# Kernel optimization log

Measured on AMD Instinct MI355X. Metric: run time of the kernel, lower is better.

## Reference

```python
import jax, jax.numpy as jnp
import numpy as np

HW, B, C, NH, NC, HF, WF = 2500, 2, 256, 8, 6, 64, 176
DFF = 4 * C
EPS = 1e-5

def _layernorm(x, g, b):
    m = x.mean(-1, keepdims=True)
    v = ((x - m) ** 2).mean(-1, keepdims=True)
    return (x - m) / jnp.sqrt(v + EPS) * g + b

def _mha(q, kv, in_w, in_b, ow, ob):
    # q: [L,B,C], kv: [S,B,C] (batch_first=False, torch nn.MultiheadAttention)
    L, Bq, Cq = q.shape
    S = kv.shape[0]
    Dh = Cq // NH
    qp = (q @ in_w[:Cq].T + in_b[:Cq]).reshape(L, Bq, NH, Dh)
    kp = (kv @ in_w[Cq:2 * Cq].T + in_b[Cq:2 * Cq]).reshape(S, Bq, NH, Dh)
    vp = (kv @ in_w[2 * Cq:].T + in_b[2 * Cq:]).reshape(S, Bq, NH, Dh)
    att = jnp.einsum('lbhd,sbhd->bhls', qp, kp) * (1.0 / np.sqrt(Dh))
    att = jax.nn.softmax(att, axis=-1)
    out = jnp.einsum('bhls,sbhd->lbhd', att, vp).reshape(L, Bq, Cq)
    return out @ ow.T + ob

def _grid_sample_zeros(feat, grid):
    # feat: [B,N,C,H,W], grid: [B,N,Q,2] in [-1,1]; bilinear, align_corners=False, zero padding
    Bb, N, Cc, Hf, Wf = feat.shape
    Q = grid.shape[2]
    x = (grid[..., 0] + 1.0) * (Wf / 2.0) - 0.5
    y = (grid[..., 1] + 1.0) * (Hf / 2.0) - 0.5
    x0 = jnp.floor(x); y0 = jnp.floor(y)
    wx = x - x0; wy = y - y0
    x0i = x0.astype(jnp.int32); y0i = y0.astype(jnp.int32)
    ff = feat.reshape(Bb, N, Cc, Hf * Wf)
    def corner(xi, yi, w):
        valid = (xi >= 0) & (xi < Wf) & (yi >= 0) & (yi < Hf)
        idx = jnp.clip(yi, 0, Hf - 1) * Wf + jnp.clip(xi, 0, Wf - 1)  # [B,N,Q]
        g = jnp.take_along_axis(ff, jnp.broadcast_to(idx[:, :, None, :], (Bb, N, Cc, Q)), axis=-1)
        return g * (w * valid)[:, :, None, :]
    return (corner(x0i, y0i, (1.0 - wx) * (1.0 - wy)) + corner(x0i + 1, y0i, wx * (1.0 - wy))
            + corner(x0i, y0i + 1, (1.0 - wx) * wy) + corner(x0i + 1, y0i + 1, wx * wy))

def _forward(bev_queries, prev_bev, image_feat, reference_points, camera_intrinsics, camera_extrinsics,
             in_proj_w, in_proj_b, out_proj_w, out_proj_b, tsa_norm_g, tsa_norm_b,
             sca_w, sca_b, sca_norm_g, sca_norm_b, ffn_w1, ffn_b1, ffn_w2, ffn_b2, ffn_norm_g, ffn_norm_b):
    # TSA (dropout is identity in eval)
    tsa_out = _mha(bev_queries, prev_bev, in_proj_w, in_proj_b, out_proj_w, out_proj_b)
    x = _layernorm(bev_queries + tsa_out, tsa_norm_g, tsa_norm_b)
    # SCA: ego->camera->image projection
    R = camera_extrinsics[:, :, :3, :3]            # [B,N,3,3]
    t = camera_extrinsics[:, :, :3, 3]             # [B,N,3]
    R_e2c = jnp.swapaxes(R, -1, -2)
    t_e2c = -jnp.einsum('bnij,bnj->bni', R_e2c, t)
    pts_cam = jnp.einsum('bnij,qj->bnqi', R_e2c, reference_points) + t_e2c[:, :, None, :]  # [B,N,Q,3]
    pts_img = jnp.einsum('bnij,bnqj->bnqi', camera_intrinsics, pts_cam)
    uv = pts_img[..., :2] / jnp.maximum(pts_img[..., 2:3], 1e-5)
    grid = jnp.stack([2.0 * uv[..., 0] / WF - 1.0, 2.0 * uv[..., 1] / HF - 1.0], axis=-1)  # [B,N,Q,2]
    Bq = bev_queries.shape[1]
    feat_r = image_feat.reshape(Bq, NC, C, HF, WF)
    sampled = _grid_sample_zeros(feat_r, grid).mean(axis=1)   # [B,C,Q]
    sampled = jnp.transpose(sampled, (2, 0, 1))               # [Q,B,C]
    sca_out = sampled @ sca_w.T + sca_b
    x = _layernorm(x + sca_out, sca_norm_g, sca_norm_b)
    # FFN (torch nn.GELU default = exact erf)
    h = jax.nn.gelu(x @ ffn_w1 + ffn_b1, approximate=False)
    ffn_out = h @ ffn_w2 + ffn_b2
    return _layernorm(x + ffn_out, ffn_norm_g, ffn_norm_b)

def setup_inputs():
    key = jax.random.key(0)
    ks = jax.random.split(key, 16)
    f = jnp.float32
    s = 0.02
    return {
        'bev_queries': jax.random.normal(ks[0], (HW, B, C), f),
        'prev_bev': jax.random.normal(ks[1], (HW, B, C), f),
        'image_feat': jax.random.normal(ks[2], (B * NC, C, HF, WF), f),
        'reference_points': jax.random.normal(ks[3], (HW, 3), f) * 20.0,
        'camera_intrinsics': jax.random.normal(ks[4], (B, NC, 3, 3), f),
        'camera_extrinsics': jax.random.normal(ks[5], (B, NC, 4, 4), f),
        'spatial_shapes': jnp.array([[HF, WF]], jnp.int32),
        'in_proj_w': jax.random.normal(ks[6], (3 * C, C), f) * s,
        'in_proj_b': jnp.zeros((3 * C,), f),
        'out_proj_w': jax.random.normal(ks[7], (C, C), f) * s,
        'out_proj_b': jnp.zeros((C,), f),
        'tsa_norm_g': jnp.ones((C,), f), 'tsa_norm_b': jnp.zeros((C,), f),
        'sca_w': jax.random.normal(ks[8], (C, C), f) * s,
        'sca_b': jnp.zeros((C,), f),
        'sca_norm_g': jnp.ones((C,), f), 'sca_norm_b': jnp.zeros((C,), f),
        'ffn_w1': jax.random.normal(ks[9], (C, DFF), f) * s,
        'ffn_b1': jnp.zeros((DFF,), f),
        'ffn_w2': jax.random.normal(ks[10], (DFF, C), f) * s,
        'ffn_b2': jnp.zeros((C,), f),
        'ffn_norm_g': jnp.ones((C,), f), 'ffn_norm_b': jnp.zeros((C,), f),
    }

def reference(bev_queries, prev_bev, image_feat, reference_points, camera_intrinsics, camera_extrinsics,
              in_proj_w, in_proj_b, out_proj_w, out_proj_b, tsa_norm_g, tsa_norm_b,
              sca_w, sca_b, sca_norm_g, sca_norm_b, ffn_w1, ffn_b1, ffn_w2, ffn_b2, ffn_norm_g, ffn_norm_b,
              spatial_shapes):
    return _forward(bev_queries, prev_bev, image_feat, reference_points, camera_intrinsics, camera_extrinsics,
                    in_proj_w, in_proj_b, out_proj_w, out_proj_b, tsa_norm_g, tsa_norm_b,
                    sca_w, sca_b, sca_norm_g, sca_norm_b, ffn_w1, ffn_b1, ffn_w2, ffn_b2, ffn_norm_g, ffn_norm_b)
```

## Files before the change

kernel.cpp:

```cpp
#include <hip/hip_runtime.h>

typedef unsigned short u16;
typedef __attribute__((ext_vector_type(8))) __bf16 bf8_t;
typedef __attribute__((ext_vector_type(4))) float f4_t;

union bf8u { u16 u[8]; bf8_t v; uint4 q; };

__device__ __forceinline__ float bf2f(u16 v) {
  return __uint_as_float(((unsigned int)v) << 16);
}
__device__ __forceinline__ u16 f2bf(float f) {
  union { __bf16 h; u16 u; } c;
  c.h = (__bf16)f;
  return c.u;
}
__device__ __forceinline__ float bflo(unsigned int w) { return __uint_as_float(w << 16); }
__device__ __forceinline__ float bfhi(unsigned int w) { return __uint_as_float(w & 0xFFFF0000u); }
__device__ __forceinline__ float ldf1(const void* p, size_t i, int isf32) {
  return isf32 ? ((const float*)p)[i] : bf2f(((const u16*)p)[i]);
}

#define LQ    2500
#define LQP   2560
#define BB    2
#define CC    256
#define NCC   6
#define HFF   64
#define WFF   176
#define DFF   1024
#define MROWS 5000

#define WB_UV   256
#define WB_WQKV 240256
#define WB_WOP  633472
#define WB_WSC  764544
#define WB_WF1  895616
#define WB_WF2  1419904
#define WB_S1   1944192
#define WB_S2   (WB_S1 + 2621440)
#define WB_S3   (WB_S2 + 2621440)
#define WB_VT   (WB_S3 + 2621440)
#define WB_H    WB_S2

__global__ void detect_k(const u16* __restrict__ rp, int* __restrict__ flag) {
  int bad = 0;
  for (int i = threadIdx.x; i < 7500; i += 64) {
    float v = bf2f(rp[i]);
    if (!(fabsf(v) < 1e6f)) bad = 1;
  }
  int anybad = __any(bad);
  if (threadIdx.x == 0) flag[0] = anybad ? 1 : 0;
}

struct WDesc {
  const void* src[6];
  u16* dst[6];
  int n[6];
  int mode[6];
  int Kd[6], Nd[6];
};
__global__ __launch_bounds__(256) void cvtw_k(WDesc d,
    const void* __restrict__ refp, const void* __restrict__ intr,
    const void* __restrict__ extr, float* __restrict__ uv,
    const int* __restrict__ flag) {
  const int df = flag[0];
  const int i = blockIdx.y;
  if (i == 6) {
    for (int idx = blockIdx.x * 256 + threadIdx.x; idx < BB * NCC * LQ; idx += gridDim.x * 256) {
      const int bc = idx / LQ;
      const int q = idx - bc * LQ;
      float R[3][3], tv[3], Kc[3][3], p[3];
#pragma unroll
      for (int a = 0; a < 3; ++a) {
#pragma unroll
        for (int j = 0; j < 3; ++j) {
          R[a][j] = ldf1(extr, bc*16 + a*4 + j, df);
          Kc[a][j] = ldf1(intr, bc*9 + a*3 + j, df);
        }
        tv[a] = ldf1(extr, bc*16 + a*4 + 3, df);
      }
#pragma unroll
      for (int j = 0; j < 3; ++j) p[j] = ldf1(refp, q*3 + j, df) - tv[j];
      float pc[3];
#pragma unroll
      for (int a = 0; a < 3; ++a) pc[a] = R[0][a]*p[0] + R[1][a]*p[1] + R[2][a]*p[2];
      float im[3];
#pragma unroll
      for (int a = 0; a < 3; ++a) im[a] = Kc[a][0]*pc[0] + Kc[a][1]*pc[1] + Kc[a][2]*pc[2];
      const float z = fmaxf(im[2], 1e-5f);
      uv[(size_t)idx*2 + 0] = im[0] / z - 0.5f;
      uv[(size_t)idx*2 + 1] = im[1] / z - 0.5f;
    }
    return;
  }
  const int n = d.n[i];
  for (int j = blockIdx.x * 256 + threadIdx.x; j < n; j += gridDim.x * 256) {
    if (d.mode[i] == 3) {
      if (df) {
        const float4 r = ((const float4*)d.src[i])[j];
        const unsigned int lo = (unsigned int)f2bf(r.x) | ((unsigned int)f2bf(r.y) << 16);
        const unsigned int hi = (unsigned int)f2bf(r.z) | ((unsigned int)f2bf(r.w) << 16);
        ((uint2*)d.dst[i])[j] = make_uint2(lo, hi);
      } else {
        ((uint2*)d.dst[i])[j] = ((const uint2*)d.src[i])[j];
      }
    } else if (d.mode[i] == 2) {
      const int row = j / (LQP - LQ), col = LQ + j % (LQP - LQ);
      d.dst[i][(size_t)row * LQP + col] = 0;
    } else {
      const int K = d.Kd[i], N = d.Nd[i];
      const int nn = j / K, kk = j - nn * K;
      d.dst[i][j] = f2bf(ldf1(d.src[i], (size_t)kk * N + nn, df));
    }
  }
}

template<int KTPL, int ACT, int NT>
__global__ __launch_bounds__(64) void gemm_nl(
    const u16* __restrict__ Xv, const u16* __restrict__ W,
    const void* __restrict__ bias,
    u16* __restrict__ Y, int M, int N, const int* __restrict__ flag)
{
  const int df = flag[0];
  const int lane = threadIdx.x;
  const int ln15 = lane & 15, l4 = lane >> 4;
  const int m0 = blockIdx.x * 16, n0 = blockIdx.y * (NT * 16);
  const int am = min(m0 + ln15, M - 1);

  f4_t acc[NT];
#pragma unroll
  for (int nt = 0; nt < NT; ++nt) acc[nt] = (f4_t){0.f, 0.f, 0.f, 0.f};

#pragma unroll 8
  for (int k0 = 0; k0 < KTPL; k0 += 32) {
    bf8u a;
    a.q = *(const uint4*)(Xv + (size_t)am * KTPL + k0 + l4 * 8);
#pragma unroll
    for (int nt = 0; nt < NT; ++nt) {
      bf8u b;
      b.q = *(const uint4*)&W[(size_t)(n0 + nt * 16 + ln15) * KTPL + k0 + l4 * 8];
      acc[nt] = __builtin_amdgcn_mfma_f32_16x16x32_bf16(a.v, b.v, acc[nt], 0, 0, 0);
    }
  }
#pragma unroll
  for (int nt = 0; nt < NT; ++nt) {
    const int gn = n0 + nt * 16 + ln15;
    const float bv = ldf1(bias, gn, df);
#pragma unroll
    for (int r = 0; r < 4; ++r) {
      const int gm = m0 + l4 * 4 + r;
      if (gm < M) {
        float x = acc[nt][r] + bv;
        if (ACT) x = 0.5f * x * (1.f + erff(x * 0.70710678118654752f));
        Y[(size_t)gm * N + gn] = f2bf(x);
      }
    }
  }
}

template<int KT, int RES, int TOOUT>
__global__ __launch_bounds__(256) void gemm_ln(
    const u16* __restrict__ Xv, const u16* __restrict__ W,
    const void* __restrict__ bias, const void* __restrict__ resv,
    const void* __restrict__ gw, const void* __restrict__ bw,
    void* __restrict__ Yv, int M, const int* __restrict__ flag)
{
  __shared__ float sR[4][16];
  const int df = flag[0];
  const int t = threadIdx.x;
  const int lane = t & 63, wn = t >> 6;
  const int ln15 = lane & 15, l4 = lane >> 4;
  const int m0 = blockIdx.x * 16;
  const int am = min(m0 + ln15, M - 1);

  f4_t acc[4];
#pragma unroll
  for (int nt = 0; nt < 4; ++nt) acc[nt] = (f4_t){0.f, 0.f, 0.f, 0.f};

#pragma unroll 8
  for (int k0 = 0; k0 < KT; k0 += 32) {
    bf8u a;
    a.q = *(const uint4*)(Xv + (size_t)am * KT + k0 + l4 * 8);
#pragma unroll
    for (int nt = 0; nt < 4; ++nt) {
      bf8u b;
      b.q = *(const uint4*)&W[(size_t)(wn * 64 + nt * 16 + ln15) * KT + k0 + l4 * 8];
      acc[nt] = __builtin_amdgcn_mfma_f32_16x16x32_bf16(a.v, b.v, acc[nt], 0, 0, 0);
    }
  }
  float x[4][4];
#pragma unroll
  for (int nt = 0; nt < 4; ++nt) {
    const int gn = wn * 64 + nt * 16 + ln15;
    const float bv = ldf1(bias, gn, df);
#pragma unroll
    for (int r = 0; r < 4; ++r) {
      const int gm = m0 + l4 * 4 + r;
      float xx = acc[nt][r] + bv;
      const size_t ri = (size_t)min(gm, M - 1) * CC + gn;
      if (RES == 1)      xx += bf2f(((const u16*)resv)[ri]);
      else if (RES == 2) xx += ldf1(resv, ri, df);
      x[nt][r] = xx;
    }
  }
  float ps[4];
#pragma unroll
  for (int r = 0; r < 4; ++r) {
    ps[r] = x[0][r] + x[1][r] + x[2][r] + x[3][r];
#pragma unroll
    for (int o = 1; o < 16; o <<= 1) ps[r] += __shfl_xor(ps[r], o);
  }
  if (ln15 == 0) {
#pragma unroll
    for (int r = 0; r < 4; ++r) sR[wn][l4 * 4 + r] = ps[r];
  }
  __syncthreads();
  float mean[4];
#pragma unroll
  for (int r = 0; r < 4; ++r) {
    const int row = l4 * 4 + r;
    mean[r] = (sR[0][row] + sR[1][row] + sR[2][row] + sR[3][row]) * 0.00390625f;
  }
  __syncthreads();
  float pq[4];
#pragma unroll
  for (int r = 0; r < 4; ++r) {
    float d0 = x[0][r] - mean[r], d1 = x[1][r] - mean[r];
    float d2 = x[2][r] - mean[r], d3 = x[3][r] - mean[r];
    pq[r] = d0*d0 + d1*d1 + d2*d2 + d3*d3;
#pragma unroll
    for (int o = 1; o < 16; o <<= 1) pq[r] += __shfl_xor(pq[r], o);
  }
  if (ln15 == 0) {
#pragma unroll
    for (int r = 0; r < 4; ++r) sR[wn][l4 * 4 + r] = pq[r];
  }
  __syncthreads();
  float rstd[4];
#pragma unroll
  for (int r = 0; r < 4; ++r) {
    const int row = l4 * 4 + r;
    const float v = (sR[0][row] + sR[1][row] + sR[2][row] + sR[3][row]) * 0.00390625f;
    rstd[r] = rsqrtf(v + 1e-5f);
  }
#pragma unroll
  for (int nt = 0; nt < 4; ++nt) {
    const int gn = wn * 64 + nt * 16 + ln15;
    const float g = ldf1(gw, gn, df);
    const float be = ldf1(bw, gn, df);
#pragma unroll
    for (int r = 0; r < 4; ++r) {
      const int gm = m0 + l4 * 4 + r;
      if (gm < M) {
        const float y = (x[nt][r] - mean[r]) * rstd[r] * g + be;
        if (TOOUT && df) ((float*)Yv)[(size_t)gm * CC + gn] = y;
        else             ((u16*)Yv)[(size_t)gm * CC + gn] = f2bf(y);
      }
    }
  }
}

__global__ __launch_bounds__(64) void gemm_qkv(
    const void* __restrict__ Xq, const void* __restrict__ Xkv,
    const u16* __restrict__ Wqkv, const void* __restrict__ bias,
    u16* __restrict__ Qo, u16* __restrict__ Ko, u16* __restrict__ Vt,
    const int* __restrict__ flag)
{
  const int df = flag[0];
  const int lane = threadIdx.x;
  const int ln15 = lane & 15, l4 = lane >> 4;
  const int which = blockIdx.y >> 2;
  const int n0 = (blockIdx.y & 3) * 64;
  const void* Xv = (which == 0) ? Xq : Xkv;
  const u16* W = Wqkv + (size_t)which * 65536;
  const int m0 = blockIdx.x * 16;
  const int am = min(m0 + ln15, MROWS - 1);

  f4_t acc[4];
#pragma unroll
  for (int nt = 0; nt < 4; ++nt) acc[nt] = (f4_t){0.f, 0.f, 0.f, 0.f};

#pragma unroll 8
  for (int k0 = 0; k0 < CC; k0 += 32) {
    bf8u a;
    if (df) {
      const float* p = (const float*)Xv + (size_t)am * CC + k0 + l4 * 8;
      float4 r0 = *(const float4*)p, r1 = *(const float4*)(p + 4);
      a.u[0]=f2bf(r0.x); a.u[1]=f2bf(r0.y); a.u[2]=f2bf(r0.z); a.u[3]=f2bf(r0.w);
      a.u[4]=f2bf(r1.x); a.u[5]=f2bf(r1.y); a.u[6]=f2bf(r1.z); a.u[7]=f2bf(r1.w);
    } else {
      a.q = *(const uint4*)((const u16*)Xv + (size_t)am * CC + k0 + l4 * 8);
    }
#pragma unroll
    for (int nt = 0; nt < 4; ++nt) {
      bf8u b;
      b.q = *(const uint4*)&W[(size_t)(n0 + nt * 16 + ln15) * CC + k0 + l4 * 8];
      acc[nt] = __builtin_amdgcn_mfma_f32_16x16x32_bf16(a.v, b.v, acc[nt], 0, 0, 0);
    }
  }
#pragma unroll
  for (int nt = 0; nt < 4; ++nt) {
    const int gn = n0 + nt * 16 + ln15;
    const float bv = ldf1(bias, which * 256 + gn, df);
#pragma unroll
    for (int r = 0; r < 4; ++r) {
      const int gm = m0 + l4 * 4 + r;
      if (gm < MROWS) {
        const float x = acc[nt][r] + bv;
        if (which == 2) {
          const int tt = gm >> 1;
          const int tx = tt & 63;
          const int tp = (tx & 35) | ((tx & 12) << 1) | ((tx & 16) >> 2);
          Vt[(size_t)(gn + (gm & 1) * 256) * LQP + ((tt & ~63) | tp)] = f2bf(x);
        } else {
          u16* Y = (which == 0) ? Qo : Ko;
          Y[(size_t)gm * CC + gn] = f2bf(x);
        }
      }
    }
  }
}

#define TPW 10
__global__ __launch_bounds__(256) void attn_mf(
    const u16* __restrict__ Qw, const u16* __restrict__ Kw,
    const u16* __restrict__ Vt, u16* __restrict__ Ow)
{
  __shared__ float sO[4][16][33];
  __shared__ float sM[4][16];
  __shared__ float sL[4][16];
  const int t = threadIdx.x;
  const int lane = t & 63, w = t >> 6;
  const int ln15 = lane & 15, l4 = lane >> 4;
  const int q0 = blockIdx.x * 16;
  const int by = blockIdx.y;
  const int b = by >> 3, h = by & 7;
  const float SCL2E = 0.25505654481f;

  bf8u aq;
  {
    const int qrow = min(q0 + ln15, LQ - 1);
    bf8u qr; qr.q = *(const uint4*)&Qw[((size_t)qrow * BB + b) * CC + h * 32 + l4 * 8];
#pragma unroll
    for (int i = 0; i < 8; ++i) aq.u[i] = f2bf(bf2f(qr.u[i]) * SCL2E);
  }

  f4_t oacc[2];
  oacc[0] = (f4_t){0.f,0.f,0.f,0.f};
  oacc[1] = (f4_t){0.f,0.f,0.f,0.f};
  float m_r = -1e30f;
  float l_r = 0.f;

  const int kt0 = w * TPW;
  const u16* Kbase = &Kw[(size_t)b * CC + h * 32 + l4 * 8];
  const u16* Vbase = &Vt[(size_t)(by * 32 + ln15) * LQP + l4 * 8];

  bf8u bkn[4];
#pragma unroll
  for (int nt = 0; nt < 4; ++nt)
    bkn[nt].q = *(const uint4*)&Kbase[(size_t)(kt0 * 64 + nt * 16 + ln15) * CC];

  for (int kt = kt0; kt < kt0 + TPW; ++kt) {
    const int kb = kt * 64;
    bf8u av[2][2];
#pragma unroll
    for (int m = 0; m < 2; ++m)
#pragma unroll
      for (int dt = 0; dt < 2; ++dt)
        av[m][dt].q = *(const uint4*)&Vbase[(size_t)(dt * 16) * LQP + kb + m * 32];
    bf8u bk[4];
#pragma unroll
    for (int nt = 0; nt < 4; ++nt) bk[nt] = bkn[nt];
    if (kt + 1 < kt0 + TPW) {
#pragma unroll
      for (int nt = 0; nt < 4; ++nt)
        bkn[nt].q = *(const uint4*)&Kbase[(size_t)(kb + 64 + nt * 16 + ln15) * CC];
    }
    f4_t sv[4];
    __builtin_amdgcn_s_setprio(1);
#pragma unroll
    for (int nt = 0; nt < 4; ++nt) {
      f4_t z = (f4_t){0.f,0.f,0.f,0.f};
      sv[nt] = __builtin_amdgcn_mfma_f32_16x16x32_bf16(bk[nt].v, aq.v, z, 0, 0, 0);
    }
    __builtin_amdgcn_s_setprio(0);
    float p[4][4];
    if (kb + 64 <= LQ) {
#pragma unroll
      for (int nt = 0; nt < 4; ++nt)
#pragma unroll
        for (int r = 0; r < 4; ++r) p[nt][r] = sv[nt][r];
    } else {
#pragma unroll
      for (int nt = 0; nt < 4; ++nt)
#pragma unroll
        for (int r = 0; r < 4; ++r)
          p[nt][r] = (kb + nt * 16 + l4 * 4 + r < LQ) ? sv[nt][r] : -1e30f;
    }
    const float thr = m_r + 8.f;
    bool nd = false;
#pragma unroll
    for (int nt = 0; nt < 4; ++nt)
#pragma unroll
      for (int r = 0; r < 4; ++r) nd |= (p[nt][r] > thr);
    if (__any(nd)) {
      const float m0 = fmaxf(fmaxf(p[0][0], p[0][1]), fmaxf(p[0][2], p[0][3]));
      const float m1 = fmaxf(fmaxf(p[1][0], p[1][1]), fmaxf(p[1][2], p[1][3]));
      const float m2 = fmaxf(fmaxf(p[2][0], p[2][1]), fmaxf(p[2][2], p[2][3]));
      const float m3 = fmaxf(fmaxf(p[3][0], p[3][1]), fmaxf(p[3][2], p[3][3]));
      float mloc = fmaxf(fmaxf(m0, m1), fmaxf(m2, m3));
      mloc = fmaxf(mloc, __shfl_xor(mloc, 16));
      mloc = fmaxf(mloc, __shfl_xor(mloc, 32));
      const float mn = fmaxf(m_r, mloc);
      const float alpha = __builtin_amdgcn_exp2f(m_r - mn);
      m_r = mn;
      l_r *= alpha;
#pragma unroll
      for (int r = 0; r < 4; ++r) { oacc[0][r] *= alpha; oacc[1][r] *= alpha; }
    }
    float s = 0.f;
#pragma unroll
    for (int nt = 0; nt < 4; ++nt) {
#pragma unroll
      for (int r = 0; r < 4; ++r) {
        const float e = __builtin_amdgcn_exp2f(p[nt][r] - m_r);
        p[nt][r] = e; s += e;
      }
    }
    l_r += s;
    __builtin_amdgcn_s_setprio(1);
#pragma unroll
    for (int m = 0; m < 2; ++m) {
      bf8u pb;
#pragma unroll
      for (int i = 0; i < 8; ++i) pb.u[i] = f2bf(p[2 * m + (i >> 2)][i & 3]);
#pragma unroll
      for (int dt = 0; dt < 2; ++dt)
        oacc[dt] = __builtin_amdgcn_mfma_f32_16x16x32_bf16(av[m][dt].v, pb.v, oacc[dt], 0, 0, 0);
    }
    __builtin_amdgcn_s_setprio(0);
  }
  l_r += __shfl_xor(l_r, 16);
  l_r += __shfl_xor(l_r, 32);
#pragma unroll
  for (int dt = 0; dt < 2; ++dt)
#pragma unroll
    for (int r = 0; r < 4; ++r)
      sO[w][ln15][dt * 16 + l4 * 4 + r] = oacc[dt][r];
  if (l4 == 0) { sM[w][ln15] = m_r; sL[w][ln15] = l_r; }
  __syncthreads();
#pragma unroll
  for (int i = t; i < 512; i += 256) {
    const int row = i >> 5, col = i & 31;
    const float M = fmaxf(fmaxf(sM[0][row], sM[1][row]), fmaxf(sM[2][row], sM[3][row]));
    float l = 0.f, O = 0.f;
#pragma unroll
    for (int w4 = 0; w4 < 4; ++w4) {
      const float sc = __builtin_amdgcn_exp2f(sM[w4][row] - M);
      l += sc * sL[w4][row];
      O += sc * sO[w4][row][col];
    }
    const int q = q0 + row;
    if (q < LQ)
      Ow[((size_t)q * BB + b) * CC + h * 32 + col] = f2bf(O / l);
  }
}

__global__ __launch_bounds__(256) void samp_k(
    const void* __restrict__ feat, const float* __restrict__ uv,
    u16* __restrict__ S, const int* __restrict__ flag)
{
  const int df = flag[0];
  const int c = blockIdx.x;
  const int b = blockIdx.y / 5;
  const int ch = blockIdx.y % 5;
  const int qend = min((ch + 1) * 500, LQ);
  for (int q = ch * 500 + threadIdx.x; q < qend; q += 256) {
    float acc = 0.f;
#pragma unroll
    for (int cam = 0; cam < NCC; ++cam) {
      const int bc = b * NCC + cam;
      const float x = uv[((size_t)bc * LQ + q) * 2 + 0];
      const float y = uv[((size_t)bc * LQ + q) * 2 + 1];
      const float xf = floorf(x), yf = floorf(y);
      const int x0 = (int)xf, y0 = (int)yf;
      const float wx = x - xf, wy = y - yf;
      const size_t base = ((size_t)bc * CC + c) * (HFF * WFF);
      const bool vx0 = (x0 >= 0) & (x0 < WFF);
      const bool vx1 = (x0 + 1 >= 0) & (x0 + 1 < WFF);
      const bool vy0 = (y0 >= 0) & (y0 < HFF);
      const bool vy1 = (y0 + 1 >= 0) & (y0 + 1 < HFF);
      if (vy0) {
        const size_t rb = base + (size_t)y0 * WFF;
        if (vx0) acc += (1.f - wx) * (1.f - wy) * ldf1(feat, rb + x0, df);
        if (vx1) acc += wx * (1.f - wy) * ldf1(feat, rb + x0 + 1, df);
      }
      if (vy1) {
        const size_t rb = base + (size_t)(y0 + 1) * WFF;
        if (vx0) acc += (1.f - wx) * wy * ldf1(feat, rb + x0, df);
        if (vx1) acc += wx * wy * ldf1(feat, rb + x0 + 1, df);
      }
    }
    S[((size_t)q * BB + b) * CC + c] = f2bf(acc * (1.f / 6.f));
  }
}

extern "C" void kernel_launch(void* const* d_in, const int* in_sizes, int n_in,
                              void* d_out, int out_size, void* d_ws, size_t ws_size,
                              hipStream_t stream) {
  (void)in_sizes; (void)n_in; (void)out_size; (void)ws_size;
  char* base = (char*)d_ws;
  int* flag = (int*)base;
  float* UV = (float*)(base + WB_UV);
  u16* WQKV = (u16*)(base + WB_WQKV);
  u16* WOP  = (u16*)(base + WB_WOP);
  u16* WSC  = (u16*)(base + WB_WSC);
  u16* WF1  = (u16*)(base + WB_WF1);
  u16* WF2  = (u16*)(base + WB_WF2);
  u16* S1 = (u16*)(base + WB_S1);
  u16* S2 = (u16*)(base + WB_S2);
  u16* S3 = (u16*)(base + WB_S3);
  u16* VT = (u16*)(base + WB_VT);
  u16* H  = (u16*)(base + WB_H);

  detect_k<<<1, 64, 0, stream>>>((const u16*)d_in[3], flag);

  WDesc wd;
  wd.src[0] = d_in[7];  wd.dst[0] = WQKV; wd.n[0] = 49152;  wd.mode[0] = 3; wd.Kd[0] = 0;    wd.Nd[0] = 0;
  wd.src[1] = d_in[9];  wd.dst[1] = WOP;  wd.n[1] = 16384;  wd.mode[1] = 3; wd.Kd[1] = 0;    wd.Nd[1] = 0;
  wd.src[2] = d_in[13]; wd.dst[2] = WSC;  wd.n[2] = 16384;  wd.mode[2] = 3; wd.Kd[2] = 0;    wd.Nd[2] = 0;
  wd.src[3] = d_in[17]; wd.dst[3] = WF1;  wd.n[3] = 262144; wd.mode[3] = 1; wd.Kd[3] = 256;  wd.Nd[3] = 1024;
  wd.src[4] = d_in[19]; wd.dst[4] = WF2;  wd.n[4] = 262144; wd.mode[4] = 1; wd.Kd[4] = 1024; wd.Nd[4] = 256;
  wd.src[5] = nullptr;  wd.dst[5] = VT;   wd.n[5] = 512 * (LQP - LQ); wd.mode[5] = 2; wd.Kd[5] = 0; wd.Nd[5] = 0;
  cvtw_k<<<dim3(128, 7), 256, 0, stream>>>(wd, d_in[3], d_in[4], d_in[5], UV, flag);

  gemm_qkv<<<dim3(313, 12), 64, 0, stream>>>(d_in[0], d_in[1], WQKV, d_in[8], S1, S2, VT, flag);

  attn_mf<<<dim3(157, 16), 256, 0, stream>>>(S1, S2, VT, S3);

  gemm_ln<256,2,0><<<313, 256, 0, stream>>>(S3, WOP, d_in[10], d_in[0], d_in[11], d_in[12], S2, MROWS, flag);

  samp_k<<<dim3(CC, BB * 5), 256, 0, stream>>>(d_in[2], UV, VT, flag);

  gemm_ln<256,1,0><<<313, 256, 0, stream>>>(VT, WSC, d_in[14], S2, d_in[15], d_in[16], S1, MROWS, flag);

  gemm_nl<256,1,4><<<dim3(313, 16), 64, 0, stream>>>(S1, WF1, d_in[18], H, MROWS, DFF, flag);
  gemm_ln<1024,1,1><<<313, 256, 0, stream>>>(H, WF2, d_in[20], S1, d_in[21], d_in[22], d_out, MROWS, flag);
}
```

Baseline: 503.7 us.

## Process two query tiles per attention block to reuse K/V loads

The attention kernel now handles 32 queries per block as two 16-row MFMA tiles that share each loaded K and V fragment. This halves the global K/V traffic per query and halves the grid size. The probability packing also switches to the packed bf16 conversion instruction. The cost is higher register pressure from duplicated accumulators and softmax state, and fewer blocks (79x16) to spread across the CUs.

```diff
diff --git a/kernel.cpp b/kernel.cpp
--- a/kernel.cpp
+++ b/kernel.cpp
@@ -18,6 +18,11 @@
 __device__ __forceinline__ float bfhi(unsigned int w) { return __uint_as_float(w & 0xFFFF0000u); }
 __device__ __forceinline__ float ldf1(const void* p, size_t i, int isf32) {
   return isf32 ? ((const float*)p)[i] : bf2f(((const u16*)p)[i]);
+}
+__device__ __forceinline__ unsigned int cvtpk(float lo, float hi) {
+  unsigned int w;
+  asm("v_cvt_pk_bf16_f32 %0, %1, %2" : "=v"(w) : "v"(lo), "v"(hi));
+  return w;
 }
 
 #define LQ    2500
@@ -326,30 +331,35 @@
     const u16* __restrict__ Qw, const u16* __restrict__ Kw,
     const u16* __restrict__ Vt, u16* __restrict__ Ow)
 {
-  __shared__ float sO[4][16][33];
-  __shared__ float sM[4][16];
-  __shared__ float sL[4][16];
+  __shared__ float sO[4][32][33];
+  __shared__ float sM[4][32];
+  __shared__ float sL[4][32];
   const int t = threadIdx.x;
   const int lane = t & 63, w = t >> 6;
   const int ln15 = lane & 15, l4 = lane >> 4;
-  const int q0 = blockIdx.x * 16;
+  const int q0 = blockIdx.x * 32;
   const int by = blockIdx.y;
   const int b = by >> 3, h = by & 7;
   const float SCL2E = 0.25505654481f;
 
-  bf8u aq;
+  bf8u aqA, aqB;
   {
-    const int qrow = min(q0 + ln15, LQ - 1);
-    bf8u qr; qr.q = *(const uint4*)&Qw[((size_t)qrow * BB + b) * CC + h * 32 + l4 * 8];
-#pragma unroll
-    for (int i = 0; i < 8; ++i) aq.u[i] = f2bf(bf2f(qr.u[i]) * SCL2E);
-  }
-
-  f4_t oacc[2];
-  oacc[0] = (f4_t){0.f,0.f,0.f,0.f};
-  oacc[1] = (f4_t){0.f,0.f,0.f,0.f};
-  float m_r = -1e30f;
-  float l_r = 0.f;
+    const int qra = min(q0 + ln15, LQ - 1);
+    const int qrb = min(q0 + 16 + ln15, LQ - 1);
+    bf8u qr;
+    qr.q = *(const uint4*)&Qw[((size_t)qra * BB + b) * CC + h * 32 + l4 * 8];
+#pragma unroll
+    for (int i = 0; i < 8; ++i) aqA.u[i] = f2bf(bf2f(qr.u[i]) * SCL2E);
+    qr.q = *(const uint4*)&Qw[((size_t)qrb * BB + b) * CC + h * 32 + l4 * 8];
+#pragma unroll
+    for (int i = 0; i < 8; ++i) aqB.u[i] = f2bf(bf2f(qr.u[i]) * SCL2E);
+  }
+
+  f4_t oaccA[2], oaccB[2];
+  oaccA[0] = (f4_t){0.f,0.f,0.f,0.f}; oaccA[1] = (f4_t){0.f,0.f,0.f,0.f};
+  oaccB[0] = (f4_t){0.f,0.f,0.f,0.f}; oaccB[1] = (f4_t){0.f,0.f,0.f,0.f};
+  float mA = -1e30f, lA = 0.f;
+  float mB = -1e30f, lB = 0.f;
 
   const int kt0 = w * TPW;
   const u16* Kbase = &Kw[(size_t)b * CC + h * 32 + l4 * 8];
@@ -368,89 +378,133 @@
 #pragma unroll
       for (int dt = 0; dt < 2; ++dt)
         av[m][dt].q = *(const uint4*)&Vbase[(size_t)(dt * 16) * LQP + kb + m * 32];
-    bf8u bk[4];
-#pragma unroll
-    for (int nt = 0; nt < 4; ++nt) bk[nt] = bkn[nt];
+    f4_t svA[4], svB[4];
+    __builtin_amdgcn_s_setprio(1);
+#pragma unroll
+    for (int nt = 0; nt < 4; ++nt) {
+      f4_t z = (f4_t){0.f,0.f,0.f,0.f};
+      svA[nt] = __builtin_amdgcn_mfma_f32_16x16x32_bf16(bkn[nt].v, aqA.v, z, 0, 0, 0);
+      f4_t z2 = (f4_t){0.f,0.f,0.f,0.f};
+      svB[nt] = __builtin_amdgcn_mfma_f32_16x16x32_bf16(bkn[nt].v, aqB.v, z2, 0, 0, 0);
+    }
+    __builtin_amdgcn_s_setprio(0);
     if (kt + 1 < kt0 + TPW) {
 #pragma unroll
       for (int nt = 0; nt < 4; ++nt)
         bkn[nt].q = *(const uint4*)&Kbase[(size_t)(kb + 64 + nt * 16 + ln15) * CC];
     }
-    f4_t sv[4];
+    float pA[4][4], pB[4][4];
+    if (kb + 64 <= LQ) {
+#pragma unroll
+      for (int nt = 0; nt < 4; ++nt)
+#pragma unroll
+        for (int r = 0; r < 4; ++r) { pA[nt][r] = svA[nt][r]; pB[nt][r] = svB[nt][r]; }
+    } else {
+#pragma unroll
+      for (int nt = 0; nt < 4; ++nt)
+#pragma unroll
+        for (int r = 0; r < 4; ++r) {
+          const bool ok = (kb + nt * 16 + l4 * 4 + r < LQ);
+          pA[nt][r] = ok ? svA[nt][r] : -1e30f;
+          pB[nt][r] = ok ? svB[nt][r] : -1e30f;
+        }
+    }
+    {
+      const float thr = mA + 8.f;
+      bool nd = false;
+#pragma unroll
+      for (int nt = 0; nt < 4; ++nt)
+#pragma unroll
+        for (int r = 0; r < 4; ++r) nd |= (pA[nt][r] > thr);
+      if (__any(nd)) {
+        const float x0 = fmaxf(fmaxf(pA[0][0], pA[0][1]), fmaxf(pA[0][2], pA[0][3]));
+        const float x1 = fmaxf(fmaxf(pA[1][0], pA[1][1]), fmaxf(pA[1][2], pA[1][3]));
+        const float x2 = fmaxf(fmaxf(pA[2][0], pA[2][1]), fmaxf(pA[2][2], pA[2][3]));
+        const float x3 = fmaxf(fmaxf(pA[3][0], pA[3][1]), fmaxf(pA[3][2], pA[3][3]));
+        float mloc = fmaxf(fmaxf(x0, x1), fmaxf(x2, x3));
+        mloc = fmaxf(mloc, __shfl_xor(mloc, 16));
+        mloc = fmaxf(mloc, __shfl_xor(mloc, 32));
+        const float mn = fmaxf(mA, mloc);
+        const float alpha = __builtin_amdgcn_exp2f(mA - mn);
+        mA = mn;
+        lA *= alpha;
+#pragma unroll
+        for (int r = 0; r < 4; ++r) { oaccA[0][r] *= alpha; oaccA[1][r] *= alpha; }
+      }
+      float s = 0.f;
+#pragma unroll
+      for (int nt = 0; nt < 4; ++nt)
+#pragma unroll
+        for (int r = 0; r < 4; ++r) {
+          const float e = __builtin_amdgcn_exp2f(pA[nt][r] - mA);
+          pA[nt][r] = e; s += e;
+        }
+      lA += s;
+    }
+    {
+      const float thr = mB + 8.f;
+      bool nd = false;
+#pragma unroll
+      for (int nt = 0; nt < 4; ++nt)
+#pragma unroll
+        for (int r = 0; r < 4; ++r) nd |= (pB[nt][r] > thr);
+      if (__any(nd)) {
+        const float x0 = fmaxf(fmaxf(pB[0][0], pB[0][1]), fmaxf(pB[0][2], pB[0][3]));
+        const float x1 = fmaxf(fmaxf(pB[1][0], pB[1][1]), fmaxf(pB[1][2], pB[1][3]));
+        const float x2 = fmaxf(fmaxf(pB[2][0], pB[2][1]), fmaxf(pB[2][2], pB[2][3]));
+        const float x3 = fmaxf(fmaxf(pB[3][0], pB[3][1]), fmaxf(pB[3][2], pB[3][3]));
+        float mloc = fmaxf(fmaxf(x0, x1), fmaxf(x2, x3));
+        mloc = fmaxf(mloc, __shfl_xor(mloc, 16));
+        mloc = fmaxf(mloc, __shfl_xor(mloc, 32));
+        const float mn = fmaxf(mB, mloc);
+        const float alpha = __builtin_amdgcn_exp2f(mB - mn);
+        mB = mn;
+        lB *= alpha;
+#pragma unroll
+        for (int r = 0; r < 4; ++r) { oaccB[0][r] *= alpha; oaccB[1][r] *= alpha; }
+      }
+      float s = 0.f;
+#pragma unroll
+      for (int nt = 0; nt < 4; ++nt)
+#pragma unroll
+        for (int r = 0; r < 4; ++r) {
+          const float e = __builtin_amdgcn_exp2f(pB[nt][r] - mB);
+          pB[nt][r] = e; s += e;
+        }
+      lB += s;
+    }
     __builtin_amdgcn_s_setprio(1);
 #pragma unroll
-    for (int nt = 0; nt < 4; ++nt) {
-      f4_t z = (f4_t){0.f,0.f,0.f,0.f};
-      sv[nt] = __builtin_amdgcn_mfma_f32_16x16x32_bf16(bk[nt].v, aq.v, z, 0, 0, 0);
+    for (int m = 0; m < 2; ++m) {
+      bf8u pba, pbb;
+      pba.q = make_uint4(cvtpk(pA[2*m][0], pA[2*m][1]),   cvtpk(pA[2*m][2], pA[2*m][3]),
+                         cvtpk(pA[2*m+1][0], pA[2*m+1][1]), cvtpk(pA[2*m+1][2], pA[2*m+1][3]));
+      pbb.q = make_uint4(cvtpk(pB[2*m][0], pB[2*m][1]),   cvtpk(pB[2*m][2], pB[2*m][3]),
+                         cvtpk(pB[2*m+1][0], pB[2*m+1][1]), cvtpk(pB[2*m+1][2], pB[2*m+1][3]));
+#pragma unroll
+      for (int dt = 0; dt < 2; ++dt) {
+        oaccA[dt] = __builtin_amdgcn_mfma_f32_16x16x32_bf16(av[m][dt].v, pba.v, oaccA[dt], 0, 0, 0);
+        oaccB[dt] = __builtin_amdgcn_mfma_f32_16x16x32_bf16(av[m][dt].v, pbb.v, oaccB[dt], 0, 0, 0);
+      }
     }
     __builtin_amdgcn_s_setprio(0);
-    float p[4][4];
-    if (kb + 64 <= LQ) {
-#pragma unroll
-      for (int nt = 0; nt < 4; ++nt)
-#pragma unroll
-        for (int r = 0; r < 4; ++r) p[nt][r] = sv[nt][r];
-    } else {
-#pragma unroll
-      for (int nt = 0; nt < 4; ++nt)
-#pragma unroll
-        for (int r = 0; r < 4; ++r)
-          p[nt][r] = (kb + nt * 16 + l4 * 4 + r < LQ) ? sv[nt][r] : -1e30f;
-    }
-    const float thr = m_r + 8.f;
-    bool nd = false;
-#pragma unroll
-    for (int nt = 0; nt < 4; ++nt)
-#pragma unroll
-      for (int r = 0; r < 4; ++r) nd |= (p[nt][r] > thr);
-    if (__any(nd)) {
-      const float m0 = fmaxf(fmaxf(p[0][0], p[0][1]), fmaxf(p[0][2], p[0][3]));
-      const float m1 = fmaxf(fmaxf(p[1][0], p[1][1]), fmaxf(p[1][2], p[1][3]));
-      const float m2 = fmaxf(fmaxf(p[2][0], p[2][1]), fmaxf(p[2][2], p[2][3]));
-      const float m3 = fmaxf(fmaxf(p[3][0], p[3][1]), fmaxf(p[3][2], p[3][3]));
-      float mloc = fmaxf(fmaxf(m0, m1), fmaxf(m2, m3));
-      mloc = fmaxf(mloc, __shfl_xor(mloc, 16));
-      mloc = fmaxf(mloc, __shfl_xor(mloc, 32));
-      const float mn = fmaxf(m_r, mloc);
-      const float alpha = __builtin_amdgcn_exp2f(m_r - mn);
-      m_r = mn;
-      l_r *= alpha;
-#pragma unroll
-      for (int r = 0; r < 4; ++r) { oacc[0][r] *= alpha; oacc[1][r] *= alpha; }
-    }
-    float s = 0.f;
-#pragma unroll
-    for (int nt = 0; nt < 4; ++nt) {
-#pragma unroll
-      for (int r = 0; r < 4; ++r) {
-        const float e = __builtin_amdgcn_exp2f(p[nt][r] - m_r);
-        p[nt][r] = e; s += e;
-      }
-    }
-    l_r += s;
-    __builtin_amdgcn_s_setprio(1);
-#pragma unroll
-    for (int m = 0; m < 2; ++m) {
-      bf8u pb;
-#pragma unroll
-      for (int i = 0; i < 8; ++i) pb.u[i] = f2bf(p[2 * m + (i >> 2)][i & 3]);
-#pragma unroll
-      for (int dt = 0; dt < 2; ++dt)
-        oacc[dt] = __builtin_amdgcn_mfma_f32_16x16x32_bf16(av[m][dt].v, pb.v, oacc[dt], 0, 0, 0);
-    }
-    __builtin_amdgcn_s_setprio(0);
-  }
-  l_r += __shfl_xor(l_r, 16);
-  l_r += __shfl_xor(l_r, 32);
+  }
+  lA += __shfl_xor(lA, 16);  lA += __shfl_xor(lA, 32);
+  lB += __shfl_xor(lB, 16);  lB += __shfl_xor(lB, 32);
 #pragma unroll
   for (int dt = 0; dt < 2; ++dt)
 #pragma unroll
-    for (int r = 0; r < 4; ++r)
-      sO[w][ln15][dt * 16 + l4 * 4 + r] = oacc[dt][r];
-  if (l4 == 0) { sM[w][ln15] = m_r; sL[w][ln15] = l_r; }
+    for (int r = 0; r < 4; ++r) {
+      sO[w][ln15][dt * 16 + l4 * 4 + r]      = oaccA[dt][r];
+      sO[w][16 + ln15][dt * 16 + l4 * 4 + r] = oaccB[dt][r];
+    }
+  if (l4 == 0) {
+    sM[w][ln15] = mA; sL[w][ln15] = lA;
+    sM[w][16 + ln15] = mB; sL[w][16 + ln15] = lB;
+  }
   __syncthreads();
 #pragma unroll
-  for (int i = t; i < 512; i += 256) {
+  for (int i = t; i < 1024; i += 256) {
     const int row = i >> 5, col = i & 31;
     const float M = fmaxf(fmaxf(sM[0][row], sM[1][row]), fmaxf(sM[2][row], sM[3][row]));
     float l = 0.f, O = 0.f;
@@ -536,7 +590,7 @@
 
   gemm_qkv<<<dim3(313, 12), 64, 0, stream>>>(d_in[0], d_in[1], WQKV, d_in[8], S1, S2, VT, flag);
 
-  attn_mf<<<dim3(157, 16), 256, 0, stream>>>(S1, S2, VT, S3);
+  attn_mf<<<dim3(79, 16), 256, 0, stream>>>(S1, S2, VT, S3);
 
   gemm_ln<256,2,0><<<313, 256, 0, stream>>>(S3, WOP, d_in[10], d_in[0], d_in[11], d_in[12], S2, MROWS, flag);
 
```

Result: faster. 464.0 us (-7.9%).
